# Optimization experiments

Hardware: AMD Instinct MI355X
Metric: run time of the kernel (lower is better)

The kernel has to match this reference:

```python
import jax, jax.numpy as jnp
import numpy as np

N, T, F_IN, H, D_FF, C_OUT = 4096, 60, 64, 128, 256, 1


def _gru_layer(x_tnf, W_ih, W_hh, b_ih, b_hh):
    # torch nn.GRU single layer; x_tnf: [T, N, in]
    def step(h, xt):
        gi = xt @ W_ih.T + b_ih          # [N, 3H]
        gh = h @ W_hh.T + b_hh
        i_r, i_z, i_n = jnp.split(gi, 3, axis=-1)
        h_r, h_z, h_n = jnp.split(gh, 3, axis=-1)
        r = jax.nn.sigmoid(i_r + h_r)
        z = jax.nn.sigmoid(i_z + h_z)
        n = jnp.tanh(i_n + r * h_n)
        h = (1.0 - z) * n + z * h
        return h, h
    h0 = jnp.zeros((x_tnf.shape[1], W_hh.shape[1]), x_tnf.dtype)
    hT, ys = jax.lax.scan(step, h0, x_tnf)
    return hT, ys


def setup_inputs() -> dict:
    key = jax.random.key(0)
    ks = jax.random.split(key, 20)
    s_in = 1.0 / np.sqrt(F_IN)
    s_h = 1.0 / np.sqrt(H)
    inp = {
        'x': jax.random.normal(ks[0], (N, T, F_IN), jnp.float32),
        'W_ih0': jax.random.normal(ks[1], (3 * H, F_IN), jnp.float32) * s_in,
        'W_hh0': jax.random.normal(ks[2], (3 * H, H), jnp.float32) * s_h,
        'b_ih0': jax.random.normal(ks[3], (3 * H,), jnp.float32) * s_h,
        'b_hh0': jax.random.normal(ks[4], (3 * H,), jnp.float32) * s_h,
        'W_ih1': jax.random.normal(ks[5], (3 * H, H), jnp.float32) * s_h,
        'W_hh1': jax.random.normal(ks[6], (3 * H, H), jnp.float32) * s_h,
        'b_ih1': jax.random.normal(ks[7], (3 * H,), jnp.float32) * s_h,
        'b_hh1': jax.random.normal(ks[8], (3 * H,), jnp.float32) * s_h,
        'Wt': jax.random.normal(ks[9], (H, H), jnp.float32) * s_h,
        'bt': jax.random.normal(ks[10], (H,), jnp.float32) * s_h,
        'a': jax.random.normal(ks[11], (2 * H, 1), jnp.float32),
        'Wfc': jax.random.normal(ks[12], (H, H), jnp.float32) * s_h,
        'bfc': jax.random.normal(ks[13], (H,), jnp.float32) * s_h,
        'Wp1': jax.random.normal(ks[14], (D_FF, H), jnp.float32) * s_h,
        'bp1': jax.random.normal(ks[15], (D_FF,), jnp.float32) * s_h,
        'Wp2': jax.random.normal(ks[16], (C_OUT, D_FF), jnp.float32) * (1.0 / np.sqrt(D_FF)),
        'bp2': jax.random.normal(ks[17], (C_OUT,), jnp.float32) * (1.0 / np.sqrt(D_FF)),
    }
    return inp


def reference(x, W_ih0, W_hh0, b_ih0, b_hh0, W_ih1, W_hh1, b_ih1, b_hh1,
              Wt, bt, a, Wfc, bfc, Wp1, bp1, Wp2, bp2):
    x_tnf = jnp.transpose(x, (1, 0, 2))  # [T, N, F]
    _, ys0 = _gru_layer(x_tnf, W_ih0, W_hh0, b_ih0, b_hh0)
    hT, _ = _gru_layer(ys0, W_ih1, W_hh1, b_ih1, b_hh1)
    hidden = hT  # out[:, -1, :], [N, H]

    # cal_attention: score[i,j] = a[:H].x_j + a[H:].x_i  (separable GAT score)
    xt = hidden @ Wt.T + bt                      # transformation(x) == transformation(y)
    a_flat = a[:, 0]
    s_j = xt @ a_flat[:H]                        # [N], contributes per-column
    s_i = xt @ a_flat[H:]                        # [N], contributes per-row
    scores = jax.nn.leaky_relu(s_i[:, None] + s_j[None, :], negative_slope=0.01)
    att = jax.nn.softmax(scores, axis=1)         # [N, N]

    hidden = att @ hidden + hidden
    hidden = jax.nn.leaky_relu(hidden @ Wfc.T + bfc, negative_slope=0.01)
    h1 = jax.nn.gelu(hidden @ Wp1.T + bp1, approximate=False)
    out = h1 @ Wp2.T + bp2                       # [N, 1]
    return jnp.squeeze(out)                      # [N]
```

## Files before the change

### kernel.cpp

```cpp
#include <hip/hip_runtime.h>
#include <cstdint>
#include <cstddef>

#define TSTEPS 60
#define NB 4096
#define HD 128

typedef __attribute__((ext_vector_type(8))) short short8;
typedef __attribute__((ext_vector_type(4))) float f32x4;

#define WS_SJ    0
#define WS_SI    16384
#define WS_HID   32768
#define WS_HTH   2129920
#define WS_HTL   3178496
#define WS_F0H   4227072
#define WS_F0L   (WS_F0H+49152)
#define WS_FR0H  (WS_F0L+49152)
#define WS_FR0L  (WS_FR0H+98304)
#define WS_FR1H  (WS_FR0L+98304)
#define WS_FR1L  (WS_FR1H+98304)
#define WS_FR2H  (WS_FR1L+98304)
#define WS_FR2L  (WS_FR2H+98304)
#define WS_BASE  (WS_FR2L+98304)
#define WS_Y0P   WS_BASE
#define WS_FULL  (WS_Y0P + 125829120ULL)

__device__ __forceinline__ float b2f(unsigned short h){ return __uint_as_float(((unsigned)h)<<16); }
__device__ __forceinline__ unsigned short f2b(float f){
  unsigned u = __float_as_uint(f);
  u = (u + 0x7FFFu + ((u>>16)&1u)) >> 16;
  return (unsigned short)u;
}
__device__ __forceinline__ float sigm(float x){ return 1.0f/(1.0f + __expf(-x)); }
__device__ __forceinline__ float tanhfast(float x){
  float xc = fminf(fmaxf(x,-15.0f),15.0f);
  float e = __expf(2.0f*xc);
  return (e-1.0f)/(e+1.0f);
}
__device__ __forceinline__ float lrelu(float x){ return x > 0.0f ? x : 0.01f*x; }
__device__ __forceinline__ float ldr1(const void* p, size_t i, int f32){
  return f32 ? ((const float*)p)[i] : b2f(((const unsigned short*)p)[i]);
}
template<bool F32>
__device__ __forceinline__ float4 ldg4c(const void* p, size_t i){
  if (F32) return *(const float4*)((const float*)p + i);
  ushort4 u = *(const ushort4*)((const unsigned short*)p + i);
  float4 f; f.x=b2f(u.x); f.y=b2f(u.y); f.z=b2f(u.z); f.w=b2f(u.w); return f;
}
__device__ __forceinline__ f32x4 f4zero(){ f32x4 v = {0.f,0.f,0.f,0.f}; return v; }
__device__ __forceinline__ void pinv(short8& v){ asm volatile("" : "+v"(v)); }

__device__ __forceinline__ void ldsbar(){
  asm volatile("s_waitcnt lgkmcnt(0)\n\ts_barrier" ::: "memory");
}

__device__ int probe_f32(const void* p, int nprobe, volatile int* s){
  if (threadIdx.x == 0) *s = 0;
  __syncthreads();
  if ((int)threadIdx.x < nprobe) {
    float v = b2f(((const unsigned short*)p)[threadIdx.x]);
    if (!(v == v) || fabsf(v) > 1e4f) *s = 1;
  }
  __syncthreads();
  int r = *s;
  __syncthreads();
  return r;
}

__global__ void diag_kernel(float* out, float code){
  int i = blockIdx.x*256 + threadIdx.x;
  if (i < 4096) out[i] = code;
}

__device__ void repack_mat(const void* src, int f32, int K, int nks,
                           unsigned short* hi, unsigned short* lo,
                           int tid, int nthr){
  int total = 384*K;
  for (int idx = tid; idx < total; idx += nthr) {
    int j = idx & 7, lane = (idx>>3)&63, t = idx>>9;
    int ks = t % nks, g = (t/nks)%3, w = t/(nks*3);
    int row = 16*(w + 8*g) + (lane & 15);
    int k   = ks*32 + ((lane>>4)<<3) + j;
    float v = f32 ? ((const float*)src)[(size_t)row*K + k]
                  : b2f(((const unsigned short*)src)[(size_t)row*K + k]);
    unsigned short h = f2b(v);
    hi[idx] = h;
    lo[idx] = f2b(v - b2f(h));
  }
}

__global__ __launch_bounds__(256) void repack_kernel(
    const void* wih0, const void* whh0, const void* wih1, const void* whh1,
    char* ws)
{
  __shared__ int sp;
  int f0 = probe_f32(wih0, 256, &sp);
  int f1 = probe_f32(whh0, 256, &sp);
  int f2 = probe_f32(wih1, 256, &sp);
  int f3 = probe_f32(whh1, 256, &sp);
  int tid  = blockIdx.x*256 + threadIdx.x;
  int nthr = gridDim.x*256;
  repack_mat(wih0, f0,  64, 2, (unsigned short*)(ws+WS_F0H),  (unsigned short*)(ws+WS_F0L),  tid, nthr);
  repack_mat(whh0, f1, 128, 4, (unsigned short*)(ws+WS_FR0H), (unsigned short*)(ws+WS_FR0L), tid, nthr);
  repack_mat(wih1, f2, 128, 4, (unsigned short*)(ws+WS_FR1H), (unsigned short*)(ws+WS_FR1L), tid, nthr);
  repack_mat(whh1, f3, 128, 4, (unsigned short*)(ws+WS_FR2H), (unsigned short*)(ws+WS_FR2L), tid, nthr);
}

#define MFMA __builtin_amdgcn_mfma_f32_16x16x32_bf16

__global__ __launch_bounds__(512) __attribute__((amdgpu_waves_per_eu(2,2)))
void gru0_kernel(const void* __restrict__ xg,
                 const void* __restrict__ bih0, const void* __restrict__ bhh0,
                 const char* __restrict__ ws, unsigned* __restrict__ y0p)
{
  __shared__ __align__(16) unsigned short xbh[2][1152], xbl[2][1152];
  __shared__ __align__(16) unsigned short hbh[2][2176], hbl[2][2176];
  __shared__ int sp;
  const int tid  = threadIdx.x;
  const int w    = tid >> 6;
  const int lane = tid & 63;
  const int ln   = lane & 15;
  const int kq   = lane >> 4;
  const int r0   = blockIdx.x * 16;

  int xf  = probe_f32(xg,   256, &sp);
  int fb0 = probe_f32(bih0, 256, &sp);
  int fh0 = probe_f32(bhh0, 256, &sp);

  const unsigned short* f0h  = (const unsigned short*)(ws+WS_F0H);
  const unsigned short* f0l  = (const unsigned short*)(ws+WS_F0L);
  const unsigned short* fr0h = (const unsigned short*)(ws+WS_FR0H);
  const unsigned short* fr0l = (const unsigned short*)(ws+WS_FR0L);

  short8 X0h[3][2], X0l[3][2];
  #pragma unroll
  for (int g = 0; g < 3; ++g)
    #pragma unroll
    for (int ks = 0; ks < 2; ++ks) {
      int fi = (w*3+g)*2 + ks;
      X0h[g][ks] = *(const short8*)&f0h[fi*512 + lane*8];
      X0l[g][ks] = *(const short8*)&f0l[fi*512 + lane*8];
      pinv(X0h[g][ks]); pinv(X0l[g][ks]);
    }

  short8 R0h[3][4], R0l[3][4];
  #pragma unroll
  for (int g = 0; g < 3; ++g)
    #pragma unroll
    for (int ks = 0; ks < 4; ++ks) {
      int fi = (w*3+g)*4 + ks;
      R0h[g][ks] = *(const short8*)&fr0h[fi*512 + lane*8];
      R0l[g][ks] = *(const short8*)&fr0l[fi*512 + lane*8];
      pinv(R0h[g][ks]); pinv(R0l[g][ks]);
    }

  const int nr = 16*w + ln;
  float brc0 = ldr1(bih0,nr,fb0)     + ldr1(bhh0,nr,fh0);
  float bzc0 = ldr1(bih0,nr+128,fb0) + ldr1(bhh0,nr+128,fh0);
  float bin0 = ldr1(bih0,nr+256,fb0);
  float bhn0 = ldr1(bhh0,nr+256,fh0);

  for (int i = tid; i < 2176; i += 512) { hbh[0][i] = 0; hbl[0][i] = 0; }
  const int xm = tid >> 5, xfc = (tid & 31)*2;
  {
    size_t base = ((size_t)(r0+xm)*TSTEPS + 0)*64 + xfc;
    float v0, v1;
    if (xf) { float2 xv = *(const float2*)((const float*)xg + base); v0 = xv.x; v1 = xv.y; }
    else { ushort2 u = *(const ushort2*)((const unsigned short*)xg + base); v0 = b2f(u.x); v1 = b2f(u.y); }
    unsigned short a0 = f2b(v0), a1 = f2b(v1);
    unsigned short l0 = f2b(v0-b2f(a0)), l1 = f2b(v1-b2f(a1));
    *(unsigned*)&xbh[0][xm*72+xfc] = (unsigned)a0 | ((unsigned)a1<<16);
    *(unsigned*)&xbl[0][xm*72+xfc] = (unsigned)l0 | ((unsigned)l1<<16);
  }
  float h0o[4] = {0.f,0.f,0.f,0.f};
  __syncthreads();

  #pragma unroll 1
  for (int t = 0; t < TSTEPS; ++t) {
    const int b0 = t & 1, b1 = b0 ^ 1;
    unsigned short pa0=0, pa1=0, pl0=0, pl1=0;
    if (t+1 < TSTEPS) {
      size_t base = ((size_t)(r0+xm)*TSTEPS + (t+1))*64 + xfc;
      float v0, v1;
      if (xf) { float2 xv = *(const float2*)((const float*)xg + base); v0 = xv.x; v1 = xv.y; }
      else { ushort2 u = *(const ushort2*)((const unsigned short*)xg + base); v0 = b2f(u.x); v1 = b2f(u.y); }
      pa0 = f2b(v0); pa1 = f2b(v1);
      pl0 = f2b(v0-b2f(pa0)); pl1 = f2b(v1-b2f(pa1));
    }

    f32x4 acc[4];
    #pragma unroll
    for (int g = 0; g < 4; ++g) acc[g] = f4zero();
    #pragma unroll
    for (int ks = 0; ks < 2; ++ks) {
      short8 axh = *(const short8*)&xbh[b0][ln*72 + ks*32 + kq*8];
      short8 axl = *(const short8*)&xbl[b0][ln*72 + ks*32 + kq*8];
      #pragma unroll
      for (int g = 0; g < 3; ++g) {
        acc[g] = MFMA(axh, X0h[g][ks], acc[g], 0,0,0);
        acc[g] = MFMA(axh, X0l[g][ks], acc[g], 0,0,0);
        acc[g] = MFMA(axl, X0h[g][ks], acc[g], 0,0,0);
      }
    }
    #pragma unroll
    for (int ks = 0; ks < 4; ++ks) {
      short8 ahh = *(const short8*)&hbh[b0][ln*136 + ks*32 + kq*8];
      short8 ahl = *(const short8*)&hbl[b0][ln*136 + ks*32 + kq*8];
      #pragma unroll
      for (int g = 0; g < 3; ++g) {
        int tgt = (g==2) ? 3 : g;
        acc[tgt] = MFMA(ahh, R0h[g][ks], acc[tgt], 0,0,0);
        acc[tgt] = MFMA(ahh, R0l[g][ks], acc[tgt], 0,0,0);
        acc[tgt] = MFMA(ahl, R0h[g][ks], acc[tgt], 0,0,0);
      }
    }
    unsigned short nh[4], nl[4];
    #pragma unroll
    for (int rg = 0; rg < 4; ++rg) {
      float r  = sigm(acc[0][rg] + brc0);
      float z  = sigm(acc[1][rg] + bzc0);
      float nn = tanhfast(acc[2][rg] + bin0 + r*(acc[3][rg] + bhn0));
      float h  = nn + z*(h0o[rg] - nn);
      h0o[rg] = h;
      unsigned short hh = f2b(h);
      nh[rg] = hh; nl[rg] = f2b(h - b2f(hh));
    }
    {
      size_t ybase = ((size_t)blockIdx.x*TSTEPS + t)*2048;
      #pragma unroll
      for (int rg = 0; rg < 4; ++rg)
        y0p[ybase + (kq*4+rg)*128 + w*16 + ln] =
            (unsigned)nh[rg] | ((unsigned)nl[rg] << 16);
    }
    #pragma unroll
    for (int rg = 0; rg < 4; ++rg) {
      int off = (kq*4+rg)*136 + w*16 + ln;
      hbh[b1][off] = nh[rg]; hbl[b1][off] = nl[rg];
    }
    if (t+1 < TSTEPS) {
      *(unsigned*)&xbh[b1][xm*72+xfc] = (unsigned)pa0 | ((unsigned)pa1<<16);
      *(unsigned*)&xbl[b1][xm*72+xfc] = (unsigned)pl0 | ((unsigned)pl1<<16);
    }
    ldsbar();
  }
}

__global__ __launch_bounds__(512) __attribute__((amdgpu_waves_per_eu(2,2)))
void gru1_kernel(const void* __restrict__ bih1, const void* __restrict__ bhh1,
                 const char* __restrict__ ws, const unsigned* __restrict__ y0p,
                 float* __restrict__ hidg,
                 unsigned short* __restrict__ hTh, unsigned short* __restrict__ hTl)
{
  __shared__ __align__(16) unsigned short wih1hL[49152];
  __shared__ __align__(16) unsigned short ybh[2][2176], ybl[2][2176];
  __shared__ __align__(16) unsigned short h1bh[2][2176], h1bl[2][2176];
  __shared__ int sp;
  const int tid  = threadIdx.x;
  const int w    = tid >> 6;
  const int lane = tid & 63;
  const int ln   = lane & 15;
  const int kq   = lane >> 4;
  const int r0   = blockIdx.x * 16;

  int fb1 = probe_f32(bih1, 256, &sp);
  int fh1 = probe_f32(bhh1, 256, &sp);

  const unsigned short* fr1h = (const unsigned short*)(ws+WS_FR1H);
  const unsigned short* fr1l = (const unsigned short*)(ws+WS_FR1L);
  const unsigned short* fr2h = (const unsigned short*)(ws+WS_FR2H);
  const unsigned short* fr2l = (const unsigned short*)(ws+WS_FR2L);

  for (int i = tid*8; i < 49152; i += 4096) {
    *(ushort4*)&wih1hL[i]   = *(const ushort4*)&fr1h[i];
    *(ushort4*)&wih1hL[i+4] = *(const ushort4*)&fr1h[i+4];
  }

  short8 W1hp[2][4];
  #pragma unroll
  for (int g = 0; g < 2; ++g)
    #pragma unroll
    for (int ks = 0; ks < 4; ++ks) {
      W1hp[g][ks] = *(const short8*)&fr1h[((w*3+g)*4+ks)*512 + lane*8];
      pinv(W1hp[g][ks]);
    }

  short8 W1l[3][4], R2h[3][4], R2l[3][4];
  #pragma unroll
  for (int g = 0; g < 3; ++g)
    #pragma unroll
    for (int ks = 0; ks < 4; ++ks) {
      int fi = (w*3+g)*4 + ks;
      W1l[g][ks] = *(const short8*)&fr1l[fi*512 + lane*8];
      R2h[g][ks] = *(const short8*)&fr2h[fi*512 + lane*8];
      R2l[g][ks] = *(const short8*)&fr2l[fi*512 + lane*8];
      pinv(W1l[g][ks]); pinv(R2h[g][ks]); pinv(R2l[g][ks]);
    }

  const int nr = 16*w + ln;
  float brc1 = ldr1(bih1,nr,fb1)     + ldr1(bhh1,nr,fh1);
  float bzc1 = ldr1(bih1,nr+128,fb1) + ldr1(bhh1,nr+128,fh1);
  float bin1 = ldr1(bih1,nr+256,fb1);
  float bhn1 = ldr1(bhh1,nr+256,fh1);

  for (int i = tid; i < 2176; i += 512) { h1bh[0][i] = 0; h1bl[0][i] = 0; }
  const int yi4 = tid*4, yrow = yi4 >> 7, ycol = yi4 & 127;
  {
    uint4 pv = *(const uint4*)&y0p[((size_t)blockIdx.x*TSTEPS + 0)*2048 + yi4];
    ushort4 vh, vl;
    vh.x=(unsigned short)(pv.x&0xffff); vl.x=(unsigned short)(pv.x>>16);
    vh.y=(unsigned short)(pv.y&0xffff); vl.y=(unsigned short)(pv.y>>16);
    vh.z=(unsigned short)(pv.z&0xffff); vl.z=(unsigned short)(pv.z>>16);
    vh.w=(unsigned short)(pv.w&0xffff); vl.w=(unsigned short)(pv.w>>16);
    *(ushort4*)&ybh[0][yrow*136+ycol] = vh;
    *(ushort4*)&ybl[0][yrow*136+ycol] = vl;
  }
  float h1o[4] = {0.f,0.f,0.f,0.f};
  __syncthreads();

  #pragma unroll 1
  for (int t = 0; t < TSTEPS; ++t) {
    const int b0 = t & 1, b1 = b0 ^ 1;
    uint4 pv = {0,0,0,0};
    if (t+1 < TSTEPS)
      pv = *(const uint4*)&y0p[((size_t)blockIdx.x*TSTEPS + (t+1))*2048 + yi4];

    f32x4 acc[4];
    #pragma unroll
    for (int g = 0; g < 4; ++g) acc[g] = f4zero();
    #pragma unroll
    for (int ks = 0; ks < 4; ++ks) {
      short8 ayh = *(const short8*)&ybh[b0][ln*136 + ks*32 + kq*8];
      short8 ayl = *(const short8*)&ybl[b0][ln*136 + ks*32 + kq*8];
      short8 a1h = *(const short8*)&h1bh[b0][ln*136 + ks*32 + kq*8];
      short8 a1l = *(const short8*)&h1bl[b0][ln*136 + ks*32 + kq*8];
      #pragma unroll
      for (int g = 0; g < 3; ++g) {
        int tgtI = (g==2) ? 2 : g;
        int tgtH = (g==2) ? 3 : g;
        short8 bh;
        if (g < 2) bh = W1hp[g][ks];
        else       bh = *(const short8*)&wih1hL[((w*3+2)*4+ks)*512 + lane*8];
        acc[tgtI] = MFMA(ayh, bh,         acc[tgtI], 0,0,0);
        acc[tgtI] = MFMA(ayh, W1l[g][ks], acc[tgtI], 0,0,0);
        acc[tgtI] = MFMA(ayl, bh,         acc[tgtI], 0,0,0);
        acc[tgtH] = MFMA(a1h, R2h[g][ks], acc[tgtH], 0,0,0);
        acc[tgtH] = MFMA(a1h, R2l[g][ks], acc[tgtH], 0,0,0);
        acc[tgtH] = MFMA(a1l, R2h[g][ks], acc[tgtH], 0,0,0);
      }
    }
    unsigned short nh[4], nl[4];
    #pragma unroll
    for (int rg = 0; rg < 4; ++rg) {
      float r  = sigm(acc[0][rg] + brc1);
      float z  = sigm(acc[1][rg] + bzc1);
      float nn = tanhfast(acc[2][rg] + bin1 + r*(acc[3][rg] + bhn1));
      float h  = nn + z*(h1o[rg] - nn);
      h1o[rg] = h;
      unsigned short hh = f2b(h);
      nh[rg] = hh; nl[rg] = f2b(h - b2f(hh));
    }
    #pragma unroll
    for (int rg = 0; rg < 4; ++rg) {
      int off = (kq*4+rg)*136 + w*16 + ln;
      h1bh[b1][off] = nh[rg]; h1bl[b1][off] = nl[rg];
    }
    if (t+1 < TSTEPS) {
      ushort4 vh, vl;
      vh.x=(unsigned short)(pv.x&0xffff); vl.x=(unsigned short)(pv.x>>16);
      vh.y=(unsigned short)(pv.y&0xffff); vl.y=(unsigned short)(pv.y>>16);
      vh.z=(unsigned short)(pv.z&0xffff); vl.z=(unsigned short)(pv.z>>16);
      vh.w=(unsigned short)(pv.w&0xffff); vl.w=(unsigned short)(pv.w>>16);
      *(ushort4*)&ybh[b1][yrow*136+ycol] = vh;
      *(ushort4*)&ybl[b1][yrow*136+ycol] = vl;
    }
    ldsbar();
  }

  {
    int c = w*16 + ln;
    #pragma unroll
    for (int rg = 0; rg < 4; ++rg)
      hidg[(size_t)(r0 + kq*4 + rg)*HD + c] = h1o[rg];
    ushort4 ph, pl;
    unsigned short* hh = (unsigned short*)&ph;
    unsigned short* ll = (unsigned short*)&pl;
    #pragma unroll
    for (int rg = 0; rg < 4; ++rg) {
      hh[rg] = f2b(h1o[rg]);
      ll[rg] = f2b(h1o[rg] - b2f(hh[rg]));
    }
    size_t o = (size_t)c*NB + r0 + kq*4;
    *(ushort4*)&hTh[o] = ph;
    *(ushort4*)&hTl[o] = pl;
  }
}

__global__ __launch_bounds__(512, 1) void gru_fb_kernel(
    const void* __restrict__ xg,
    const void* __restrict__ bih0, const void* __restrict__ bhh0,
    const void* __restrict__ bih1, const void* __restrict__ bhh1,
    const char* __restrict__ ws, float* __restrict__ hidg,
    unsigned short* __restrict__ hTh, unsigned short* __restrict__ hTl)
{
  __shared__ __align__(16) unsigned short wih0L[49152];
  __shared__ __align__(16) unsigned short xhi[1152], xlo[1152];
  __shared__ __align__(16) unsigned short h0hi[2176], h0lo[2176];
  __shared__ __align__(16) unsigned short h1hi[2176], h1lo[2176];
  __shared__ int sp;
  const int tid  = threadIdx.x;
  const int w    = tid >> 6;
  const int lane = tid & 63;
  const int ln   = lane & 15;
  const int kq   = lane >> 4;
  const int r0   = blockIdx.x * 16;

  int xf  = probe_f32(xg,   256, &sp);
  int fb0 = probe_f32(bih0, 256, &sp);
  int fh0 = probe_f32(bhh0, 256, &sp);
  int fb1 = probe_f32(bih1, 256, &sp);
  int fh1 = probe_f32(bhh1, 256, &sp);

  const unsigned short* f0h  = (const unsigned short*)(ws+WS_F0H);
  const unsigned short* f0l  = (const unsigned short*)(ws+WS_F0L);
  const unsigned short* fr0h = (const unsigned short*)(ws+WS_FR0H);
  const unsigned short* fr0l = (const unsigned short*)(ws+WS_FR0L);
  const unsigned short* fr1h = (const unsigned short*)(ws+WS_FR1H);
  const unsigned short* fr1l = (const unsigned short*)(ws+WS_FR1L);
  const unsigned short* fr2h = (const unsigned short*)(ws+WS_FR2H);
  const unsigned short* fr2l = (const unsigned short*)(ws+WS_FR2L);

  for (int i = tid*8; i < 24576; i += 4096) {
    *(ushort4*)&wih0L[i]         = *(const ushort4*)&f0h[i];
    *(ushort4*)&wih0L[i+4]       = *(const ushort4*)&f0h[i+4];
    *(ushort4*)&wih0L[24576+i]   = *(const ushort4*)&f0l[i];
    *(ushort4*)&wih0L[24576+i+4] = *(const ushort4*)&f0l[i+4];
  }
  short8 R0h[3][4], R1h[3][4], R2h[3][4];
  #pragma unroll
  for (int g = 0; g < 3; ++g)
    #pragma unroll
    for (int ks = 0; ks < 4; ++ks) {
      int fi = (w*3+g)*4 + ks;
      R0h[g][ks] = *(const short8*)&fr0h[fi*512 + lane*8];
      R1h[g][ks] = *(const short8*)&fr1h[fi*512 + lane*8];
      R2h[g][ks] = *(const short8*)&fr2h[fi*512 + lane*8];
      pinv(R0h[g][ks]); pinv(R1h[g][ks]); pinv(R2h[g][ks]);
    }
  const int nr = 16*w + ln;
  float brc0 = ldr1(bih0,nr,fb0)     + ldr1(bhh0,nr,fh0);
  float bzc0 = ldr1(bih0,nr+128,fb0) + ldr1(bhh0,nr+128,fh0);
  float bin0 = ldr1(bih0,nr+256,fb0);
  float bhn0 = ldr1(bhh0,nr+256,fh0);
  float brc1 = ldr1(bih1,nr,fb1)     + ldr1(bhh1,nr,fh1);
  float bzc1 = ldr1(bih1,nr+128,fb1) + ldr1(bhh1,nr+128,fh1);
  float bin1 = ldr1(bih1,nr+256,fb1);
  float bhn1 = ldr1(bhh1,nr+256,fh1);

  for (int i = tid; i < 2176; i += 512) {
    h0hi[i] = 0; h0lo[i] = 0; h1hi[i] = 0; h1lo[i] = 0;
  }
  float h0o[4] = {0.f,0.f,0.f,0.f};
  float h1o[4] = {0.f,0.f,0.f,0.f};
  __syncthreads();

  #pragma unroll 1
  for (int t = 0; t < TSTEPS; ++t) {
    {
      int i0 = tid*2, m = i0 >> 6, f = i0 & 63;
      size_t base = ((size_t)(r0+m)*TSTEPS + t)*64 + f;
      float v0, v1;
      if (xf) { float2 xv = *(const float2*)((const float*)xg + base); v0 = xv.x; v1 = xv.y; }
      else { ushort2 u = *(const ushort2*)((const unsigned short*)xg + base); v0 = b2f(u.x); v1 = b2f(u.y); }
      unsigned short a0 = f2b(v0), a1 = f2b(v1);
      xhi[m*72+f] = a0;              xhi[m*72+f+1] = a1;
      xlo[m*72+f] = f2b(v0-b2f(a0)); xlo[m*72+f+1] = f2b(v1-b2f(a1));
    }
    __syncthreads();
    f32x4 acc[4];
    #pragma unroll
    for (int g = 0; g < 4; ++g) acc[g] = f4zero();
    #pragma unroll
    for (int ks = 0; ks < 2; ++ks) {
      short8 axh = *(const short8*)&xhi[ln*72 + ks*32 + kq*8];
      short8 axl = *(const short8*)&xlo[ln*72 + ks*32 + kq*8];
      #pragma unroll
      for (int g = 0; g < 3; ++g) {
        int fi = (w*3+g)*2 + ks;
        short8 bh = *(const short8*)&wih0L[fi*512 + lane*8];
        short8 bl = *(const short8*)&wih0L[24576 + fi*512 + lane*8];
        acc[g] = MFMA(axh, bh, acc[g], 0,0,0);
        acc[g] = MFMA(axh, bl, acc[g], 0,0,0);
        acc[g] = MFMA(axl, bh, acc[g], 0,0,0);
      }
    }
    #pragma unroll
    for (int ks = 0; ks < 4; ++ks) {
      short8 ahh = *(const short8*)&h0hi[ln*136 + ks*32 + kq*8];
      short8 ahl = *(const short8*)&h0lo[ln*136 + ks*32 + kq*8];
      #pragma unroll
      for (int g = 0; g < 3; ++g) {
        int tgt = (g==2) ? 3 : g;
        short8 bl = *(const short8*)&fr0l[((w*3+g)*4+ks)*512 + lane*8];
        acc[tgt] = MFMA(ahh, R0h[g][ks], acc[tgt], 0,0,0);
        acc[tgt] = MFMA(ahh, bl,         acc[tgt], 0,0,0);
        acc[tgt] = MFMA(ahl, R0h[g][ks], acc[tgt], 0,0,0);
      }
    }
    unsigned short nh[4], nl[4];
    #pragma unroll
    for (int rg = 0; rg < 4; ++rg) {
      float r  = sigm(acc[0][rg] + brc0);
      float z  = sigm(acc[1][rg] + bzc0);
      float nn = tanhfast(acc[2][rg] + bin0 + r*(acc[3][rg] + bhn0));
      float h  = nn + z*(h0o[rg] - nn);
      h0o[rg] = h;
      unsigned short hh = f2b(h);
      nh[rg] = hh; nl[rg] = f2b(h - b2f(hh));
    }
    __syncthreads();
    #pragma unroll
    for (int rg = 0; rg < 4; ++rg) {
      int off = (kq*4+rg)*136 + w*16 + ln;
      h0hi[off] = nh[rg]; h0lo[off] = nl[rg];
    }
    __syncthreads();
    #pragma unroll
    for (int g = 0; g < 4; ++g) acc[g] = f4zero();
    #pragma unroll
    for (int ks = 0; ks < 4; ++ks) {
      short8 ayh = *(const short8*)&h0hi[ln*136 + ks*32 + kq*8];
      short8 ayl = *(const short8*)&h0lo[ln*136 + ks*32 + kq*8];
      short8 a1h = *(const short8*)&h1hi[ln*136 + ks*32 + kq*8];
      short8 a1l = *(const short8*)&h1lo[ln*136 + ks*32 + kq*8];
      #pragma unroll
      for (int g = 0; g < 3; ++g) {
        int tgtI = (g==2) ? 2 : g;
        int tgtH = (g==2) ? 3 : g;
        short8 blI = *(const short8*)&fr1l[((w*3+g)*4+ks)*512 + lane*8];
        short8 blH = *(const short8*)&fr2l[((w*3+g)*4+ks)*512 + lane*8];
        acc[tgtI] = MFMA(ayh, R1h[g][ks], acc[tgtI], 0,0,0);
        acc[tgtI] = MFMA(ayh, blI,        acc[tgtI], 0,0,0);
        acc[tgtI] = MFMA(ayl, R1h[g][ks], acc[tgtI], 0,0,0);
        acc[tgtH] = MFMA(a1h, R2h[g][ks], acc[tgtH], 0,0,0);
        acc[tgtH] = MFMA(a1h, blH,        acc[tgtH], 0,0,0);
        acc[tgtH] = MFMA(a1l, R2h[g][ks], acc[tgtH], 0,0,0);
      }
    }
    #pragma unroll
    for (int rg = 0; rg < 4; ++rg) {
      float r  = sigm(acc[0][rg] + brc1);
      float z  = sigm(acc[1][rg] + bzc1);
      float nn = tanhfast(acc[2][rg] + bin1 + r*(acc[3][rg] + bhn1));
      float h  = nn + z*(h1o[rg] - nn);
      h1o[rg] = h;
      unsigned short hh = f2b(h);
      nh[rg] = hh; nl[rg] = f2b(h - b2f(hh));
    }
    __syncthreads();
    #pragma unroll
    for (int rg = 0; rg < 4; ++rg) {
      int off = (kq*4+rg)*136 + w*16 + ln;
      h1hi[off] = nh[rg]; h1lo[off] = nl[rg];
    }
  }
  {
    int c = w*16 + ln;
    #pragma unroll
    for (int rg = 0; rg < 4; ++rg)
      hidg[(size_t)(r0 + kq*4 + rg)*HD + c] = h1o[rg];
    ushort4 ph, pl;
    unsigned short* hh = (unsigned short*)&ph;
    unsigned short* ll = (unsigned short*)&pl;
    #pragma unroll
    for (int rg = 0; rg < 4; ++rg) {
      hh[rg] = f2b(h1o[rg]);
      ll[rg] = f2b(h1o[rg] - b2f(hh[rg]));
    }
    size_t o = (size_t)c*NB + r0 + kq*4;
    *(ushort4*)&hTh[o] = ph;
    *(ushort4*)&hTl[o] = pl;
  }
}

template<bool WT32>
__device__ void sprep_body(
    const float* hidg, const void* wt, const void* bt, const void* a,
    int f_bt, int f_a, float* sjg, float* sig, float* hL, float* redb)
{
  const int tid = threadIdx.x;
  const int r0  = blockIdx.x * 16;
  for (int i = tid; i < 2048; i += 256) hL[i] = hidg[(size_t)r0*128 + i];
  __syncthreads();
  const int r = tid >> 4, cg = tid & 15, c0 = cg*8;
  float sjp = 0.f, sip = 0.f;
  #pragma unroll 1
  for (int cc = 0; cc < 8; ++cc) {
    int cI = c0 + cc;
    float acc = ldr1(bt, cI, f_bt);
    #pragma unroll 4
    for (int kq = 0; kq < 32; ++kq) {
      int k = kq*4;
      float4 wv = ldg4c<WT32>(wt, (size_t)cI*128 + k);
      float4 h = *(const float4*)&hL[r*128 + k];
      acc += wv.x*h.x + wv.y*h.y + wv.z*h.z + wv.w*h.w;
    }
    sjp += acc * ldr1(a, cI, f_a);
    sip += acc * ldr1(a, cI + 128, f_a);
  }
  redb[(r*16+cg)*2]   = sjp;
  redb[(r*16+cg)*2+1] = sip;
  __syncthreads();
  if (tid < 32) {
    int r2 = tid >> 1, wh = tid & 1;
    float s = 0.f;
    for (int g = 0; g < 16; ++g) s += redb[(r2*16+g)*2 + wh];
    if (wh == 0) sjg[r0+r2] = s; else sig[r0+r2] = s;
  }
}

__global__ __launch_bounds__(256) void sprep_kernel(
    const float* hidg, const void* wt, const void* bt, const void* a,
    float* sjg, float* sig)
{
  __shared__ float hL[2048];
  __shared__ float redb[512];
  __shared__ int sp;
  int f_wt = probe_f32(wt, 256, &sp);
  int f_bt = probe_f32(bt, 128, &sp);
  int f_a  = probe_f32(a,  256, &sp);
  if (f_wt) sprep_body<true >(hidg, wt, bt, a, f_bt, f_a, sjg, sig, hL, redb);
  else      sprep_body<false>(hidg, wt, bt, a, f_bt, f_a, sjg, sig, hL, redb);
}

template<bool PW32>
__device__ void attn_body(
    const float* sjg, const float* sig, const float* hidg,
    const unsigned short* hTh, const unsigned short* hTl,
    const void* wfc, const void* bfc, const void* wp1, const void* bp1,
    const void* wp2, const void* bp2,
    int f_bfc, int f_bp1, int f_wp2, float* outg,
    float* sjs, unsigned short* Pbuf, float* Obuf, float* redm,
    float* siL, float* miL, float* Zb)
{
  unsigned short* Phi = Pbuf;
  unsigned short* Plo = Pbuf + 8320;
  const int tid = threadIdx.x;
  const int w = tid >> 6, lane = tid & 63, ln = lane & 15, kq = lane >> 4;
  const int r0 = blockIdx.x * 16;

  for (int i = tid; i < 4096; i += 512) sjs[i] = sjg[i];
  __syncthreads();
  float mx = -1e30f;
  for (int i = tid; i < 4096; i += 512) mx = fmaxf(mx, sjs[i]);
  redm[tid] = mx;
  __syncthreads();
  for (int s = 256; s > 0; s >>= 1) {
    if (tid < s) redm[tid] = fmaxf(redm[tid], redm[tid+s]);
    __syncthreads();
  }
  if (tid < 16) {
    float si = sig[r0 + tid];
    siL[tid] = si;
    miL[tid] = lrelu(si + redm[0]);
  }
  __syncthreads();

  float zp[16];
  #pragma unroll
  for (int i = 0; i < 16; ++i) zp[i] = 0.f;
  f32x4 accO = f4zero();
  const int col = w*16 + ln;

  #pragma unroll 1
  for (int ch = 0; ch < 8; ++ch) {
    {
      float sjv = sjs[ch*512 + tid];
      #pragma unroll
      for (int i = 0; i < 16; ++i) {
        float v = lrelu(siL[i] + sjv);
        float p = __expf(v - miL[i]);
        zp[i] += p;
        unsigned short hh = f2b(p);
        Phi[i*520 + tid] = hh;
        Plo[i*520 + tid] = f2b(p - b2f(hh));
      }
    }
    __syncthreads();
    #pragma unroll
    for (int ks = 0; ks < 16; ++ks) {
      short8 Ah = *(const short8*)&Phi[ln*520 + ks*32 + kq*8];
      short8 Al = *(const short8*)&Plo[ln*520 + ks*32 + kq*8];
      size_t bo = (size_t)col*NB + ch*512 + ks*32 + kq*8;
      short8 Bh = *(const short8*)&hTh[bo];
      short8 Bl = *(const short8*)&hTl[bo];
      accO = MFMA(Ah, Bh, accO, 0,0,0);
      accO = MFMA(Ah, Bl, accO, 0,0,0);
      accO = MFMA(Al, Bh, accO, 0,0,0);
    }
    __syncthreads();
  }

  #pragma unroll
  for (int rg = 0; rg < 4; ++rg)
    Obuf[(kq*4+rg)*128 + col] = accO[rg];

  float* zarr = (float*)Pbuf;
  #pragma unroll
  for (int i = 0; i < 16; ++i) zarr[i*512 + tid] = zp[i];
  __syncthreads();
  {
    int row = tid >> 5, t0 = tid & 31;
    float s = 0.f;
    #pragma unroll
    for (int k = 0; k < 16; ++k) s += zarr[row*512 + t0 + 32*k];
    redm[row*32 + t0] = s;
  }
  __syncthreads();
  if (tid < 16) {
    float s = 0.f;
    for (int g = 0; g < 32; ++g) s += redm[tid*32 + g];
    Zb[tid] = s;
  }
  __syncthreads();

  {
    int e0 = tid*4, row = e0 >> 7, c = e0 & 127;
    float zi = Zb[row];
    #pragma unroll
    for (int e = 0; e < 4; ++e)
      Obuf[e0+e] = Obuf[e0+e]/zi + hidg[(size_t)(r0+row)*128 + c + e];
  }
  __syncthreads();

  float* h3f = sjs;
  {
    int o0 = tid*4, row = o0 >> 7, c = o0 & 127;
    #pragma unroll 1
    for (int e = 0; e < 4; ++e) {
      int cI = c + e;
      float acc = ldr1(bfc, cI, f_bfc);
      #pragma unroll 4
      for (int k4 = 0; k4 < 32; ++k4) {
        int k = k4*4;
        float4 wv = ldg4c<PW32>(wfc, (size_t)cI*128 + k);
        float4 h = *(const float4*)&Obuf[row*128 + k];
        acc += wv.x*h.x + wv.y*h.y + wv.z*h.z + wv.w*h.w;
      }
      h3f[row*128 + cI] = lrelu(acc);
    }
  }
  __syncthreads();

  float* h1f = (float*)Pbuf;
  {
    int o0 = tid*8, row = o0 >> 8, c = o0 & 255;
    #pragma unroll 1
    for (int e = 0; e < 8; ++e) {
      int cI = c + e;
      float acc = ldr1(bp1, cI, f_bp1);
      #pragma unroll 4
      for (int k4 = 0; k4 < 32; ++k4) {
        int k = k4*4;
        float4 wv = ldg4c<PW32>(wp1, (size_t)cI*128 + k);
        float4 h = *(const float4*)&h3f[row*128 + k];
        acc += wv.x*h.x + wv.y*h.y + wv.z*h.z + wv.w*h.w;
      }
      h1f[row*256 + cI] = 0.5f*acc*(1.0f + erff(acc*0.70710678118f));
    }
  }
  __syncthreads();

  {
    int row = tid >> 5, t0 = tid & 31;
    float s = 0.f;
    #pragma unroll
    for (int k = 0; k < 8; ++k) {
      int cI = t0 + 32*k;
      s += h1f[row*256 + cI] * ldr1(wp2, cI, f_wp2);
    }
    redm[row*32 + t0] = s;
  }
  __syncthreads();
  if (tid < 16) {
    float acc = ldr1(bp2, 0, f_bp1);
    for (int g = 0; g < 32; ++g) acc += redm[tid*32 + g];
    outg[r0 + tid] = acc;
  }
}

__global__ __launch_bounds__(512) void attn_kernel(
    const float* sjg, const float* sig, const float* hidg,
    const unsigned short* hTh, const unsigned short* hTl,
    const void* wfc, const void* bfc, const void* wp1, const void* bp1,
    const void* wp2, const void* bp2, float* outg)
{
  __shared__ float sjs[4096];
  __shared__ __align__(16) unsigned short Pbuf[16640];
  __shared__ float Obuf[2048];
  __shared__ float redm[512];
  __shared__ float siL[16], miL[16], Zb[16];
  __shared__ int sp;
  int f_wfc = probe_f32(wfc, 256, &sp);
  int f_bfc = probe_f32(bfc, 128, &sp);
  int f_bp1 = probe_f32(bp1, 256, &sp);
  int f_wp2 = probe_f32(wp2, 256, &sp);
  if (f_wfc) attn_body<true >(sjg, sig, hidg, hTh, hTl, wfc, bfc, wp1, bp1,
                              wp2, bp2, f_bfc, f_bp1, f_wp2, outg,
                              sjs, Pbuf, Obuf, redm, siL, miL, Zb);
  else       attn_body<false>(sjg, sig, hidg, hTh, hTl, wfc, bfc, wp1, bp1,
                              wp2, bp2, f_bfc, f_bp1, f_wp2, outg,
                              sjs, Pbuf, Obuf, redm, siL, miL, Zb);
}

extern "C" void kernel_launch(void* const* d_in, const int* in_sizes, int n_in,
                              void* d_out, int out_size, void* d_ws, size_t ws_size,
                              hipStream_t stream)
{
  float* out = (float*)d_out;
  const int expected[18] = {15728640,24576,49152,384,384,49152,49152,384,384,
                            16384,128,256,16384,128,32768,256,256,1};
  int bad = 0;
  if (n_in != 18 || out_size != 4096) bad = 1600;
  else for (int i = 0; i < 18; ++i) if (in_sizes[i] != expected[i]) { bad = 1600; break; }
  if (!bad && ws_size < (size_t)WS_BASE) bad = 1664;
  if (bad) { diag_kernel<<<16, 256, 0, stream>>>(out, (float)bad); return; }

  char* ws = (char*)d_ws;
  float*          sj  = (float*)(ws + WS_SJ);
  float*          si  = (float*)(ws + WS_SI);
  float*          hid = (float*)(ws + WS_HID);
  unsigned short* hTh = (unsigned short*)(ws + WS_HTH);
  unsigned short* hTl = (unsigned short*)(ws + WS_HTL);

  repack_kernel<<<256, 256, 0, stream>>>(d_in[1], d_in[2], d_in[5], d_in[6], ws);
  if (ws_size >= WS_FULL) {
    unsigned* y0p = (unsigned*)(ws + WS_Y0P);
    gru0_kernel<<<256, 512, 0, stream>>>(d_in[0], d_in[3], d_in[4], ws, y0p);
    gru1_kernel<<<256, 512, 0, stream>>>(d_in[7], d_in[8], ws, y0p,
                                         hid, hTh, hTl);
  } else {
    gru_fb_kernel<<<256, 512, 0, stream>>>(d_in[0], d_in[3], d_in[4],
                                           d_in[7], d_in[8], ws, hid, hTh, hTl);
  }
  sprep_kernel<<<256, 256, 0, stream>>>(hid, d_in[9], d_in[10], d_in[11], sj, si);
  attn_kernel<<<256, 512, 0, stream>>>(sj, si, hid, hTh, hTl,
                                       d_in[12], d_in[13], d_in[14], d_in[15],
                                       d_in[16], d_in[17], out);
}
```

Measured before the change: 594.4 us.

## Software-pipeline GRU0 input projection and double-buffer attention P tiles

In the first GRU layer, the input-projection MFMAs for step t+1 now run at the end of step t, after the new hidden state is written. The x prefetch distance grows to two steps so these MFMAs come off the serial recurrence critical path. In the attention kernel, the P tile buffer is doubled so the exp/probability generation for the next chunk overlaps the MFMA accumulation of the current chunk, removing one barrier per chunk. This costs more LDS in the attention kernel and more live registers (accX) in the GRU kernel.

```diff
diff --git a/kernel.cpp b/kernel.cpp
--- a/kernel.cpp
+++ b/kernel.cpp
@@ -163,25 +163,41 @@
 
   for (int i = tid; i < 2176; i += 512) { hbh[0][i] = 0; hbl[0][i] = 0; }
   const int xm = tid >> 5, xfc = (tid & 31)*2;
-  {
-    size_t base = ((size_t)(r0+xm)*TSTEPS + 0)*64 + xfc;
+  #pragma unroll
+  for (int tt = 0; tt < 2; ++tt) {
+    size_t base = ((size_t)(r0+xm)*TSTEPS + tt)*64 + xfc;
     float v0, v1;
     if (xf) { float2 xv = *(const float2*)((const float*)xg + base); v0 = xv.x; v1 = xv.y; }
     else { ushort2 u = *(const ushort2*)((const unsigned short*)xg + base); v0 = b2f(u.x); v1 = b2f(u.y); }
     unsigned short a0 = f2b(v0), a1 = f2b(v1);
     unsigned short l0 = f2b(v0-b2f(a0)), l1 = f2b(v1-b2f(a1));
-    *(unsigned*)&xbh[0][xm*72+xfc] = (unsigned)a0 | ((unsigned)a1<<16);
-    *(unsigned*)&xbl[0][xm*72+xfc] = (unsigned)l0 | ((unsigned)l1<<16);
+    *(unsigned*)&xbh[tt][xm*72+xfc] = (unsigned)a0 | ((unsigned)a1<<16);
+    *(unsigned*)&xbl[tt][xm*72+xfc] = (unsigned)l0 | ((unsigned)l1<<16);
   }
   float h0o[4] = {0.f,0.f,0.f,0.f};
   __syncthreads();
+
+  f32x4 accX[3];
+  #pragma unroll
+  for (int g = 0; g < 3; ++g) accX[g] = f4zero();
+  #pragma unroll
+  for (int ks = 0; ks < 2; ++ks) {
+    short8 axh = *(const short8*)&xbh[0][ln*72 + ks*32 + kq*8];
+    short8 axl = *(const short8*)&xbl[0][ln*72 + ks*32 + kq*8];
+    #pragma unroll
+    for (int g = 0; g < 3; ++g) {
+      accX[g] = MFMA(axh, X0h[g][ks], accX[g], 0,0,0);
+      accX[g] = MFMA(axh, X0l[g][ks], accX[g], 0,0,0);
+      accX[g] = MFMA(axl, X0h[g][ks], accX[g], 0,0,0);
+    }
+  }
 
   #pragma unroll 1
   for (int t = 0; t < TSTEPS; ++t) {
     const int b0 = t & 1, b1 = b0 ^ 1;
     unsigned short pa0=0, pa1=0, pl0=0, pl1=0;
-    if (t+1 < TSTEPS) {
-      size_t base = ((size_t)(r0+xm)*TSTEPS + (t+1))*64 + xfc;
+    if (t+2 < TSTEPS) {
+      size_t base = ((size_t)(r0+xm)*TSTEPS + (t+2))*64 + xfc;
       float v0, v1;
       if (xf) { float2 xv = *(const float2*)((const float*)xg + base); v0 = xv.x; v1 = xv.y; }
       else { ushort2 u = *(const ushort2*)((const unsigned short*)xg + base); v0 = b2f(u.x); v1 = b2f(u.y); }
@@ -190,19 +206,7 @@
     }
 
     f32x4 acc[4];
-    #pragma unroll
-    for (int g = 0; g < 4; ++g) acc[g] = f4zero();
-    #pragma unroll
-    for (int ks = 0; ks < 2; ++ks) {
-      short8 axh = *(const short8*)&xbh[b0][ln*72 + ks*32 + kq*8];
-      short8 axl = *(const short8*)&xbl[b0][ln*72 + ks*32 + kq*8];
-      #pragma unroll
-      for (int g = 0; g < 3; ++g) {
-        acc[g] = MFMA(axh, X0h[g][ks], acc[g], 0,0,0);
-        acc[g] = MFMA(axh, X0l[g][ks], acc[g], 0,0,0);
-        acc[g] = MFMA(axl, X0h[g][ks], acc[g], 0,0,0);
-      }
-    }
+    acc[0] = accX[0]; acc[1] = accX[1]; acc[2] = accX[2]; acc[3] = f4zero();
     #pragma unroll
     for (int ks = 0; ks < 4; ++ks) {
       short8 ahh = *(const short8*)&hbh[b0][ln*136 + ks*32 + kq*8];
@@ -238,9 +242,24 @@
       int off = (kq*4+rg)*136 + w*16 + ln;
       hbh[b1][off] = nh[rg]; hbl[b1][off] = nl[rg];
     }
+    if (t+2 < TSTEPS) {
+      *(unsigned*)&xbh[b0][xm*72+xfc] = (unsigned)pa0 | ((unsigned)pa1<<16);
+      *(unsigned*)&xbl[b0][xm*72+xfc] = (unsigned)pl0 | ((unsigned)pl1<<16);
+    }
     if (t+1 < TSTEPS) {
-      *(unsigned*)&xbh[b1][xm*72+xfc] = (unsigned)pa0 | ((unsigned)pa1<<16);
-      *(unsigned*)&xbl[b1][xm*72+xfc] = (unsigned)pl0 | ((unsigned)pl1<<16);
+      #pragma unroll
+      for (int g = 0; g < 3; ++g) accX[g] = f4zero();
+      #pragma unroll
+      for (int ks = 0; ks < 2; ++ks) {
+        short8 axh = *(const short8*)&xbh[b1][ln*72 + ks*32 + kq*8];
+        short8 axl = *(const short8*)&xbl[b1][ln*72 + ks*32 + kq*8];
+        #pragma unroll
+        for (int g = 0; g < 3; ++g) {
+          accX[g] = MFMA(axh, X0h[g][ks], accX[g], 0,0,0);
+          accX[g] = MFMA(axh, X0l[g][ks], accX[g], 0,0,0);
+          accX[g] = MFMA(axl, X0h[g][ks], accX[g], 0,0,0);
+        }
+      }
     }
     ldsbar();
   }
@@ -643,8 +662,6 @@
     float* sjs, unsigned short* Pbuf, float* Obuf, float* redm,
     float* siL, float* miL, float* Zb)
 {
-  unsigned short* Phi = Pbuf;
-  unsigned short* Plo = Pbuf + 8320;
   const int tid = threadIdx.x;
   const int w = tid >> 6, lane = tid & 63, ln = lane & 15, kq = lane >> 4;
   const int r0 = blockIdx.x * 16;
@@ -672,21 +689,30 @@
   f32x4 accO = f4zero();
   const int col = w*16 + ln;
 
+  #define GENP(CH, BASE)                                                    \
+    {                                                                       \
+      unsigned short* Phi_ = (BASE);                                        \
+      unsigned short* Plo_ = (BASE) + 8320;                                 \
+      float sjv = sjs[(CH)*512 + tid];                                      \
+      _Pragma("unroll")                                                     \
+      for (int i = 0; i < 16; ++i) {                                        \
+        float v = lrelu(siL[i] + sjv);                                      \
+        float p = __expf(v - miL[i]);                                       \
+        zp[i] += p;                                                         \
+        unsigned short hh = f2b(p);                                         \
+        Phi_[i*520 + tid] = hh;                                             \
+        Plo_[i*520 + tid] = f2b(p - b2f(hh));                               \
+      }                                                                     \
+    }
+
+  GENP(0, Pbuf);
+  __syncthreads();
+
   #pragma unroll 1
   for (int ch = 0; ch < 8; ++ch) {
-    {
-      float sjv = sjs[ch*512 + tid];
-      #pragma unroll
-      for (int i = 0; i < 16; ++i) {
-        float v = lrelu(siL[i] + sjv);
-        float p = __expf(v - miL[i]);
-        zp[i] += p;
-        unsigned short hh = f2b(p);
-        Phi[i*520 + tid] = hh;
-        Plo[i*520 + tid] = f2b(p - b2f(hh));
-      }
-    }
-    __syncthreads();
+    const int b = ch & 1;
+    unsigned short* Phi = Pbuf + b*16640;
+    unsigned short* Plo = Phi + 8320;
     #pragma unroll
     for (int ks = 0; ks < 16; ++ks) {
       short8 Ah = *(const short8*)&Phi[ln*520 + ks*32 + kq*8];
@@ -698,8 +724,10 @@
       accO = MFMA(Ah, Bl, accO, 0,0,0);
       accO = MFMA(Al, Bh, accO, 0,0,0);
     }
+    if (ch < 7) GENP(ch+1, Pbuf + (b^1)*16640);
     __syncthreads();
   }
+  #undef GENP
 
   #pragma unroll
   for (int rg = 0; rg < 4; ++rg)
@@ -796,7 +824,7 @@
     const void* wp2, const void* bp2, float* outg)
 {
   __shared__ float sjs[4096];
-  __shared__ __align__(16) unsigned short Pbuf[16640];
+  __shared__ __align__(16) unsigned short Pbuf[33280];
   __shared__ float Obuf[2048];
   __shared__ float redm[512];
   __shared__ float siL[16], miL[16], Zb[16];
```

Result: no change. 590.5 us (-0.6%).
